# Kernel optimization log

Measured on AMD Instinct MI355X. Metric: run time of the kernel, lower is better.

The kernel has to match this reference:

```python
import jax, jax.numpy as jnp
import numpy as np

B, T, D, H, L, P = 256, 96, 64, 256, 5, 14
H2 = 2 * H   # decoder hidden
O = D        # output_size must equal input_size (decoder feeds its own output back)


def setup_inputs() -> dict:
    key = jax.random.key(0)
    ks = iter(jax.random.split(key, 32))
    s = 0.08  # weight scale to keep gates out of saturation
    rn = lambda shape, sc=s: jax.random.normal(next(ks), shape, jnp.float32) * sc
    return dict(
        x=rn((B, T, D), 1.0),
        # encoder: bidirectional, layer 0 input=D, layers 1..4 input=2H
        enc_Wih0=rn((2, 4 * H, D)), enc_Whh0=rn((2, 4 * H, H)),
        enc_bih0=rn((2, 4 * H)), enc_bhh0=rn((2, 4 * H)),
        enc_Wih=rn((L - 1, 2, 4 * H, 2 * H)), enc_Whh=rn((L - 1, 2, 4 * H, H)),
        enc_bih=rn((L - 1, 2, 4 * H)), enc_bhh=rn((L - 1, 2, 4 * H)),
        # decoder: unidirectional, hidden=2H, layer 0 input=D, layers 1..4 input=2H
        dec_Wih0=rn((4 * H2, D)), dec_Whh0=rn((4 * H2, H2)),
        dec_bih0=rn((4 * H2,)), dec_bhh0=rn((4 * H2,)),
        dec_Wih=rn((L - 1, 4 * H2, H2)), dec_Whh=rn((L - 1, 4 * H2, H2)),
        dec_bih=rn((L - 1, 4 * H2)), dec_bhh=rn((L - 1, 4 * H2)),
        fc_W=rn((O, H2)), fc_b=rn((O,)),
    )


def _lstm_cell(x, h, c, Wih, Whh, bih, bhh):
    # PyTorch gate order: i, f, g, o
    g = x @ Wih.T + h @ Whh.T + (bih + bhh)
    i, f, gg, o = jnp.split(g, 4, axis=-1)
    c = jax.nn.sigmoid(f) * c + jax.nn.sigmoid(i) * jnp.tanh(gg)
    h = jax.nn.sigmoid(o) * jnp.tanh(c)
    return h, c


def _scan_dir(xs, Wih, Whh, bih, bhh, reverse):
    # xs: (T, B, Din); returns per-step hidden (T,B,Hn) + final (h, c)
    Bn, Hn = xs.shape[1], Whh.shape[-1]
    z = jnp.zeros((Bn, Hn), xs.dtype)

    def step(carry, xt):
        h, c = carry
        h, c = _lstm_cell(xt, h, c, Wih, Whh, bih, bhh)
        return (h, c), h

    (hT, cT), hs = jax.lax.scan(step, (z, z), xs, reverse=reverse)
    return hs, hT, cT


def _forward(x, enc_Wih0, enc_Whh0, enc_bih0, enc_bhh0,
             enc_Wih, enc_Whh, enc_bih, enc_bhh,
             dec_Wih0, dec_Whh0, dec_bih0, dec_bhh0,
             dec_Wih, dec_Whh, dec_bih, dec_bhh, fc_W, fc_b):
    xs = jnp.swapaxes(x, 0, 1)  # (T, B, D)
    inp = xs
    h_fin, c_fin = [], []
    for l in range(L):
        if l == 0:
            Wih, Whh, bih, bhh = enc_Wih0, enc_Whh0, enc_bih0, enc_bhh0
        else:
            Wih, Whh, bih, bhh = enc_Wih[l - 1], enc_Whh[l - 1], enc_bih[l - 1], enc_bhh[l - 1]
        hs_f, hTf, cTf = _scan_dir(inp, Wih[0], Whh[0], bih[0], bhh[0], False)
        hs_b, hTb, cTb = _scan_dir(inp, Wih[1], Whh[1], bih[1], bhh[1], True)
        inp = jnp.concatenate([hs_f, hs_b], axis=-1)  # (T, B, 2H)
        # matches h_n.view(L,2,B,H).transpose(1,2).view(L,B,2H): per layer [fwd, bwd]
        h_fin.append(jnp.concatenate([hTf, hTb], axis=-1))
        c_fin.append(jnp.concatenate([cTf, cTb], axis=-1))
    h0 = jnp.stack(h_fin)  # (L, B, 2H)
    c0 = jnp.stack(c_fin)

    dec_params = [(dec_Wih0, dec_Whh0, dec_bih0, dec_bhh0)] + \
                 [(dec_Wih[l], dec_Whh[l], dec_bih[l], dec_bhh[l]) for l in range(L - 1)]

    def dec_step(carry, _):
        h, c, xt = carry
        z = xt
        nh, nc = [], []
        for l, (Wih, Whh, bih, bhh) in enumerate(dec_params):
            hl, cl = _lstm_cell(z, h[l], c[l], Wih, Whh, bih, bhh)
            z = hl
            nh.append(hl); nc.append(cl)
        out = z @ fc_W.T + fc_b  # (B, O); fed back as next decoder input
        return (jnp.stack(nh), jnp.stack(nc), out), out

    _, outs = jax.lax.scan(dec_step, (h0, c0, x[:, -1, :]), None, length=P)
    return jnp.swapaxes(outs, 0, 1)  # (B, P, O)


def reference(x, enc_Wih0, enc_Whh0, enc_bih0, enc_bhh0,
              enc_Wih, enc_Whh, enc_bih, enc_bhh,
              dec_Wih0, dec_Whh0, dec_bih0, dec_bhh0,
              dec_Wih, dec_Whh, dec_bih, dec_bhh, fc_W, fc_b):
    return _forward(x, enc_Wih0, enc_Whh0, enc_bih0, enc_bhh0,
                    enc_Wih, enc_Whh, enc_bih, enc_bhh,
                    dec_Wih0, dec_Whh0, dec_bih0, dec_bhh0,
                    dec_Wih, dec_Whh, dec_bih, dec_bhh, fc_W, fc_b)
```

## Files before the change

kernel.cpp:

```cpp
#include <hip/hip_runtime.h>

typedef _Float16 f16;
using half8 = __attribute__((ext_vector_type(8))) _Float16;
using half4 = __attribute__((ext_vector_type(4))) _Float16;
using f32x4 = __attribute__((ext_vector_type(4))) float;

#define DEV __device__ __forceinline__
#define LD8(p) (*(const half8*)(const void*)(p))

DEV f32x4 mfma16(half8 a, half8 b, f32x4 c) {
  return __builtin_amdgcn_mfma_f32_16x16x32_f16(a, b, c, 0, 0, 0);
}
DEV float sigf(float x) { return 1.f / (1.f + __expf(-x)); }
DEV float tanhf2(float x) { float e = __expf(2.f * x); return 1.f - 2.f / (e + 1.f); }

static const size_t OFF_WIH0   = 0;
static const size_t OFF_WIH14  = 262144;
static const size_t OFF_WHH    = 8650752;
static const size_t OFF_WDEC0  = 13893632;
static const size_t OFF_WDEC14 = 16252928;
static const size_t OFF_WFC    = 33030144;
static const size_t OFF_X16    = 33095680;
static const size_t OFF_SEQA   = 36241408;
static const size_t OFF_SEQB   = 61407232;
static const size_t OFF_XG     = 86573056;
static const size_t OFF_HBUF   = 187236352;
static const size_t OFF_FLAGS  = 187760640;
static const size_t OFF_DHDB   = 188284928;
static const size_t OFF_DCST   = 190906368;
static const size_t OFF_ZFC    = 193527808;

__global__ __launch_bounds__(256) void prep(
    const float* __restrict__ x,
    const float* __restrict__ eWih0, const float* __restrict__ eWhh0,
    const float* __restrict__ eWih,  const float* __restrict__ eWhh,
    const float* __restrict__ dWih0, const float* __restrict__ dWhh0,
    const float* __restrict__ dWih,  const float* __restrict__ dWhh,
    const float* __restrict__ fcW,   char* __restrict__ ws)
{
  f16* wih0   = (f16*)(ws + OFF_WIH0);
  f16* wih14  = (f16*)(ws + OFF_WIH14);
  f16* whhf   = (f16*)(ws + OFF_WHH);
  f16* wdec0  = (f16*)(ws + OFF_WDEC0);
  f16* wdec14 = (f16*)(ws + OFF_WDEC14);
  f16* wfc    = (f16*)(ws + OFF_WFC);
  f16* x16    = (f16*)(ws + OFF_X16);
  f16* zfc    = (f16*)(ws + OFF_ZFC);
  int* flags  = (int*)(ws + OFF_FLAGS);
  const size_t total = 18137344;
  for (size_t i = (size_t)blockIdx.x * blockDim.x + threadIdx.x; i < total;
       i += (size_t)gridDim.x * blockDim.x) {
    size_t j = i;
    if (j < 131072) { wih0[j] = (f16)eWih0[j]; continue; }
    j -= 131072;
    if (j < 4194304) { wih14[j] = (f16)eWih[j]; continue; }
    j -= 4194304;
    if (j < 2621440) {
      size_t l = j >> 19, i2 = j & 524287;
      int d   = (int)(i2 >> 18);
      int uo  = (int)((i2 >> 15) & 7);
      int tile= (int)((i2 >> 14) & 1);
      int g   = (int)((i2 >> 12) & 3);
      int kc  = (int)((i2 >> 9) & 7);
      int lnv = (int)((i2 >> 3) & 63);
      int e   = (int)(i2 & 7);
      int unit = uo * 32 + tile * 16 + (lnv & 15);
      int k = kc * 32 + (lnv >> 4) * 8 + e;
      int row = g * 256 + unit;
      float v = (l == 0) ? eWhh0[((size_t)d * 1024 + row) * 256 + k]
                         : eWhh[((((l - 1) * 2 + (size_t)d) * 1024) + row) * 256 + k];
      whhf[j] = (f16)v;
      continue;
    }
    j -= 2621440;
    if (j < 1179648) {
      size_t r = j / 576, c = j % 576;
      wdec0[j] = (f16)((c < 64) ? dWih0[r * 64 + c] : dWhh0[r * 512 + (c - 64)]);
      continue;
    }
    j -= 1179648;
    if (j < 8388608) {
      size_t l = j >> 21, rem = j & 2097151;
      size_t r = rem >> 10, c = rem & 1023;
      wdec14[j] = (f16)((c < 512) ? dWih[(l * 2048 + r) * 512 + c]
                                  : dWhh[(l * 2048 + r) * 512 + (c - 512)]);
      continue;
    }
    j -= 8388608;
    if (j < 32768) { wfc[j] = (f16)fcW[j]; continue; }
    j -= 32768;
    if (j < 1572864) {
      size_t t = j >> 14, rem = j & 16383;
      size_t b = rem >> 6, d = rem & 63;
      x16[j] = (f16)x[(b * 96 + t) * 64 + d];
      continue;
    }
    j -= 1572864;
    if (j < 16384) {
      size_t b = j >> 6, d = j & 63;
      zfc[b * 512 + d] = (f16)x[(b * 96 + 95) * 64 + d];
      continue;
    }
    j -= 16384;
    flags[j] = 0;
  }
}

__global__ __launch_bounds__(256) void gemm_xg(
    const f16* __restrict__ A, int K, const f16* __restrict__ W,
    const float* __restrict__ bih, const float* __restrict__ bhh,
    f16* __restrict__ xg)
{
  __shared__ __align__(16) f16 As[128 * 32];
  __shared__ __align__(16) f16 Ws[128 * 32];
  const int dir = blockIdx.y >> 3;
  const int cb  = (blockIdx.y & 7) * 128;
  const int rb  = blockIdx.x * 128;
  const int tid = threadIdx.x;
  const int wv = tid >> 6, ln = tid & 63;
  const int wr = wv >> 1, wc = wv & 1;
  const f16* Wd = W + (size_t)dir * 1024 * K;

  f32x4 acc[4][4];
#pragma unroll
  for (int m = 0; m < 4; m++)
#pragma unroll
    for (int n = 0; n < 4; n++) acc[m][n] = (f32x4){0.f, 0.f, 0.f, 0.f};

  const int sr = tid >> 1;
  const int sk = (tid & 1) * 16;
  const int nk = K >> 5;
  for (int kt = 0; kt < nk; ++kt) {
    half8 va0 = LD8(&A[(size_t)(rb + sr) * K + kt * 32 + sk]);
    half8 va1 = LD8(&A[(size_t)(rb + sr) * K + kt * 32 + sk + 8]);
    half8 vw0 = LD8(&Wd[(size_t)(cb + sr) * K + kt * 32 + sk]);
    half8 vw1 = LD8(&Wd[(size_t)(cb + sr) * K + kt * 32 + sk + 8]);
    *(half8*)&As[sr * 32 + sk] = va0;
    *(half8*)&As[sr * 32 + sk + 8] = va1;
    *(half8*)&Ws[sr * 32 + sk] = vw0;
    *(half8*)&Ws[sr * 32 + sk + 8] = vw1;
    __syncthreads();
    half8 af[4], bf[4];
#pragma unroll
    for (int m = 0; m < 4; m++)
      af[m] = LD8(&As[(wr * 64 + m * 16 + (ln & 15)) * 32 + (ln >> 4) * 8]);
#pragma unroll
    for (int n = 0; n < 4; n++)
      bf[n] = LD8(&Ws[(wc * 64 + n * 16 + (ln & 15)) * 32 + (ln >> 4) * 8]);
#pragma unroll
    for (int m = 0; m < 4; m++)
#pragma unroll
      for (int n = 0; n < 4; n++) acc[m][n] = mfma16(af[m], bf[n], acc[m][n]);
    __syncthreads();
  }
#pragma unroll
  for (int n = 0; n < 4; n++) {
    const int col = cb + wc * 64 + n * 16 + (ln & 15);
    const float bsum = bih[dir * 1024 + col] + bhh[dir * 1024 + col];
    const int c16 = (cb + wc * 64 + n * 16) >> 4;
#pragma unroll
    for (int m = 0; m < 4; m++) {
      const int r16 = (rb + wr * 64 + m * 16) >> 4;
      half4 h;
#pragma unroll
      for (int r = 0; r < 4; r++) h[r] = (f16)(acc[m][n][r] + bsum);
      *(half4*)&xg[(((size_t)dir * 1536 + r16) * 64 + c16) * 256 + ln * 4] = h;
    }
  }
}

__global__ __launch_bounds__(128) void enc_layer(
    const f16* __restrict__ xg, const f16* __restrict__ whhf,
    f16* __restrict__ hbuf, int* __restrict__ flags,
    f16* __restrict__ seqo, f16* __restrict__ hfin, float* __restrict__ cfin,
    int layer)
{
  const int bb = blockIdx.x;
  const int d = blockIdx.y >> 3, uo = blockIdx.y & 7;
  const int tid = threadIdx.x;
  const int wv = tid >> 6, ln = tid & 63;
  const int lc = ln & 15, lk = ln >> 4;

  __shared__ __align__(16) f16 wL[32768];
  __shared__ __align__(16) f16 hB[16 * 36];

  const f16* wsrc = whhf + (size_t)(d * 8 + uo) * 32768;
#pragma unroll 4
  for (int i = 0; i < 32; i++)
    *(half8*)&wL[(i * 128 + tid) * 8] = LD8(&wsrc[(size_t)(i * 128 + tid) * 8]);
  __syncthreads();

  int* gflags = &flags[(bb * 2 + d) * 8];
  int* myflag = &gflags[uo];
  const f16* hgrp = hbuf + (size_t)(bb * 2 + d) * 8192;
  f16* hown = hbuf + (size_t)((bb * 2 + d) * 8 + uo) * 1024;
  const int base = layer * 96;
  const int rowbase = bb * 16;
  const int cu = uo * 32 + wv * 16 + lc;
  const int erow = tid >> 3, eu8 = tid & 7;

  f32x4 cst = (f32x4){0.f, 0.f, 0.f, 0.f};

  for (int t = 0; t < 96; ++t) {
    const int tt = d ? 95 - t : t;
    const int par = (t - 1) & 1, par2 = t & 1;
    const int r16 = tt * 16 + bb;
    half4 xv[4];
#pragma unroll
    for (int g = 0; g < 4; g++)
      xv[g] = *(const half4*)&xg[(((size_t)d * 1536 + r16) * 64 +
                                  (g * 16 + uo * 2 + wv)) * 256 + ln * 4];
    unsigned long long q[8][2];
    if (t > 0) {
      if (tid == 0) {
        unsigned spin = 0;
        for (;;) {
          int mn = 0x7fffffff;
#pragma unroll
          for (int p = 0; p < 8; p++) {
            int f = __hip_atomic_load(&gflags[p], __ATOMIC_RELAXED,
                                      __HIP_MEMORY_SCOPE_AGENT);
            mn = (f < mn) ? f : mn;
          }
          if (mn >= base + t || ++spin > 100000u) break;
          __builtin_amdgcn_s_sleep(1);
        }
      }
      __syncthreads();
#pragma unroll
      for (int j = 0; j < 8; j++) {
        const f16* p = hgrp + (size_t)(j * 2 + par) * 512 + lc * 32 + lk * 8;
        q[j][0] = __hip_atomic_load((const unsigned long long*)p,
                                    __ATOMIC_RELAXED, __HIP_MEMORY_SCOPE_AGENT);
        q[j][1] = __hip_atomic_load((const unsigned long long*)(p + 4),
                                    __ATOMIC_RELAXED, __HIP_MEMORY_SCOPE_AGENT);
      }
    }
    f32x4 acc[4];
#pragma unroll
    for (int g = 0; g < 4; g++)
      acc[g] = (f32x4){(float)xv[g][0], (float)xv[g][1],
                       (float)xv[g][2], (float)xv[g][3]};
    if (t > 0) {
#pragma unroll
      for (int j = 0; j < 8; j++) {
        union { unsigned long long uq[2]; half8 h; } u;
        u.uq[0] = q[j][0]; u.uq[1] = q[j][1];
#pragma unroll
        for (int g = 0; g < 4; g++) {
          half8 b = *(const half8*)&wL[(size_t)(((wv * 4 + g) * 8 + j) * 64 + ln) * 8];
          acc[g] = mfma16(u.h, b, acc[g]);
        }
      }
    }
    f16 hv[4];
#pragma unroll
    for (int r = 0; r < 4; r++) {
      float gi = sigf(acc[0][r]);
      float gf = sigf(acc[1][r]);
      float gg = tanhf2(acc[2][r]);
      float go = sigf(acc[3][r]);
      float cn = gf * cst[r] + gi * gg;
      cst[r] = cn;
      hv[r] = (f16)(go * tanhf2(cn));
    }
#pragma unroll
    for (int r = 0; r < 4; r++)
      hB[(lk * 4 + r) * 36 + wv * 16 + lc] = hv[r];
    __syncthreads();
    unsigned long long v = *(const unsigned long long*)&hB[erow * 36 + eu8 * 4];
    __hip_atomic_store((unsigned long long*)&hown[par2 * 512 + erow * 32 + eu8 * 4],
                       v, __ATOMIC_RELAXED, __HIP_MEMORY_SCOPE_AGENT);
    asm volatile("s_waitcnt vmcnt(0)" ::: "memory");
    __syncthreads();
    if (tid == 0)
      __hip_atomic_store(myflag, base + t + 1, __ATOMIC_RELAXED,
                         __HIP_MEMORY_SCOPE_AGENT);
    *(unsigned long long*)&seqo[(size_t)tt * 131072 +
        (size_t)(rowbase + erow) * 512 + d * 256 + uo * 32 + eu8 * 4] = v;
    if (t == 95) {
      *(unsigned long long*)&hfin[(size_t)(rowbase + erow) * 512 +
                                  d * 256 + uo * 32 + eu8 * 4] = v;
#pragma unroll
      for (int r = 0; r < 4; r++)
        cfin[(size_t)(rowbase + lk * 4 + r) * 512 + d * 256 + cu] = cst[r];
    }
  }
}

__global__ __launch_bounds__(128) void dec_step(
    const f16* __restrict__ A0, int K0, const f16* __restrict__ A1,
    const f16* __restrict__ W, int Kt,
    const float* __restrict__ bih, const float* __restrict__ bhh,
    float* __restrict__ cst, f16* __restrict__ h1)
{
  const int u0 = blockIdx.y * 32;
  const int rb = blockIdx.x * 64;
  const int wv = threadIdx.x >> 6, ln = threadIdx.x & 63;
  const int lc = ln & 15, lk = ln >> 4;
  const int cu = u0 + wv * 16 + lc;
  f32x4 acc[4][4];
#pragma unroll
  for (int g = 0; g < 4; g++) {
    float b = bih[g * 512 + cu] + bhh[g * 512 + cu];
#pragma unroll
    for (int rr = 0; rr < 4; rr++) acc[rr][g] = (f32x4){b, b, b, b};
  }
  const int K0c = K0 >> 5, Ktc = Kt >> 5;
  for (int kc = 0; kc < Ktc; kc++) {
    const f16* Ap; int ko;
    if (kc < K0c) { Ap = A0; ko = kc * 32; }
    else          { Ap = A1; ko = (kc - K0c) * 32; }
    half8 b[4];
#pragma unroll
    for (int g = 0; g < 4; g++)
      b[g] = LD8(&W[(size_t)(g * 512 + cu) * Kt + kc * 32 + lk * 8]);
#pragma unroll
    for (int rr = 0; rr < 4; rr++) {
      half8 a = LD8(&Ap[(size_t)(rb + rr * 16 + lc) * 512 + ko + lk * 8]);
#pragma unroll
      for (int g = 0; g < 4; g++) acc[rr][g] = mfma16(a, b[g], acc[rr][g]);
    }
  }
#pragma unroll
  for (int rr = 0; rr < 4; rr++) {
#pragma unroll
    for (int r = 0; r < 4; r++) {
      const int row = rb + rr * 16 + lk * 4 + r;
      float gi = sigf(acc[rr][0][r]);
      float gf = sigf(acc[rr][1][r]);
      float gg = tanhf2(acc[rr][2][r]);
      float go = sigf(acc[rr][3][r]);
      float cp = cst[(size_t)row * 512 + cu];
      float cn = gf * cp + gi * gg;
      cst[(size_t)row * 512 + cu] = cn;
      h1[(size_t)row * 512 + cu] = (f16)(go * tanhf2(cn));
    }
  }
}

__global__ __launch_bounds__(64) void fc_kernel(
    const f16* __restrict__ hin, const f16* __restrict__ Wf,
    const float* __restrict__ bf, float* __restrict__ out,
    f16* __restrict__ zfc, int s)
{
  const int rb = blockIdx.x * 16;
  const int ln = threadIdx.x;
  f32x4 acc[4];
#pragma unroll
  for (int n = 0; n < 4; n++) acc[n] = (f32x4){0.f, 0.f, 0.f, 0.f};
#pragma unroll
  for (int kc = 0; kc < 16; kc++) {
    half8 a = LD8(&hin[(size_t)(rb + (ln & 15)) * 512 + kc * 32 + (ln >> 4) * 8]);
#pragma unroll
    for (int n = 0; n < 4; n++) {
      half8 b = LD8(&Wf[(size_t)(n * 16 + (ln & 15)) * 512 + kc * 32 + (ln >> 4) * 8]);
      acc[n] = mfma16(a, b, acc[n]);
    }
  }
#pragma unroll
  for (int n = 0; n < 4; n++) {
    const int col = n * 16 + (ln & 15);
    const float bb = bf[col];
#pragma unroll
    for (int r = 0; r < 4; r++) {
      const int row = rb + (ln >> 4) * 4 + r;
      float v = acc[n][r] + bb;
      out[(size_t)row * 896 + s * 64 + col] = v;
      zfc[(size_t)row * 512 + col] = (f16)v;
    }
  }
}

extern "C" void kernel_launch(void* const* d_in, const int* in_sizes, int n_in,
                              void* d_out, int out_size, void* d_ws, size_t ws_size,
                              hipStream_t stream) {
  char* ws = (char*)d_ws;
  const float* x     = (const float*)d_in[0];
  const float* eWih0 = (const float*)d_in[1];
  const float* eWhh0 = (const float*)d_in[2];
  const float* ebih0 = (const float*)d_in[3];
  const float* ebhh0 = (const float*)d_in[4];
  const float* eWih  = (const float*)d_in[5];
  const float* eWhh  = (const float*)d_in[6];
  const float* ebih  = (const float*)d_in[7];
  const float* ebhh  = (const float*)d_in[8];
  const float* dWih0 = (const float*)d_in[9];
  const float* dWhh0 = (const float*)d_in[10];
  const float* dbih0 = (const float*)d_in[11];
  const float* dbhh0 = (const float*)d_in[12];
  const float* dWih  = (const float*)d_in[13];
  const float* dWhh  = (const float*)d_in[14];
  const float* dbih  = (const float*)d_in[15];
  const float* dbhh  = (const float*)d_in[16];
  const float* fcW   = (const float*)d_in[17];
  const float* fcb   = (const float*)d_in[18];

  f16* xg    = (f16*)(ws + OFF_XG);
  f16* hbuf  = (f16*)(ws + OFF_HBUF);
  int* flags = (int*)(ws + OFF_FLAGS);
  f16* dhdb  = (f16*)(ws + OFF_DHDB);
  float* dcst = (float*)(ws + OFF_DCST);
  f16* zfc   = (f16*)(ws + OFF_ZFC);
  f16* seqA  = (f16*)(ws + OFF_SEQA);
  f16* seqB  = (f16*)(ws + OFF_SEQB);

  prep<<<dim3(2048), dim3(256), 0, stream>>>(x, eWih0, eWhh0, eWih, eWhh,
                                             dWih0, dWhh0, dWih, dWhh, fcW, ws);

  for (int l = 0; l < 5; ++l) {
    const f16* Ain = (l == 0) ? (f16*)(ws + OFF_X16) : ((l & 1) ? seqA : seqB);
    const int K = (l == 0) ? 64 : 512;
    const f16* Wih = (l == 0) ? (f16*)(ws + OFF_WIH0)
                              : (f16*)(ws + OFF_WIH14) + (size_t)(l - 1) * 2 * 1024 * 512;
    const float* bi = (l == 0) ? ebih0 : ebih + (size_t)(l - 1) * 2048;
    const float* bh = (l == 0) ? ebhh0 : ebhh + (size_t)(l - 1) * 2048;
    gemm_xg<<<dim3(192, 16), dim3(256), 0, stream>>>(Ain, K, Wih, bi, bh, xg);

    const f16* whhf_l = (f16*)(ws + OFF_WHH) + (size_t)l * 524288;
    f16* so = (l & 1) ? seqB : seqA;
    enc_layer<<<dim3(16, 16), dim3(128), 0, stream>>>(
        xg, whhf_l, hbuf, flags, so,
        dhdb + (size_t)l * 131072, dcst + (size_t)l * 131072, l);
  }

  for (int s = 0; s < 14; ++s) {
    const int p = s & 1;
    for (int l = 0; l < 5; ++l) {
      dec_step<<<dim3(4, 16), dim3(128), 0, stream>>>(
          (l == 0) ? zfc : dhdb + (size_t)(p ^ 1) * 655360 + (size_t)(l - 1) * 131072,
          (l == 0) ? 64 : 512,
          dhdb + (size_t)p * 655360 + (size_t)l * 131072,
          (l == 0) ? (f16*)(ws + OFF_WDEC0)
                   : (f16*)(ws + OFF_WDEC14) + (size_t)(l - 1) * 2048 * 1024,
          (l == 0) ? 576 : 1024,
          (l == 0) ? dbih0 : dbih + (size_t)(l - 1) * 2048,
          (l == 0) ? dbhh0 : dbhh + (size_t)(l - 1) * 2048,
          dcst + (size_t)l * 131072,
          dhdb + (size_t)(p ^ 1) * 655360 + (size_t)l * 131072);
    }
    fc_kernel<<<dim3(16), dim3(64), 0, stream>>>(
        dhdb + (size_t)(p ^ 1) * 655360 + 4 * 131072, (f16*)(ws + OFF_WFC), fcb,
        (float*)d_out, zfc, s);
  }
}
```

Measured before the change: 3.863 ms.

## Replace flag-based step barrier with tagged hidden-state words in encoder

The encoder recurrent kernel stops publishing a per-block flag after each timestep and spinning on peer flags. Instead, every f16 hidden value is stored in a 32-bit word whose high half carries the timestep tag, and consumers spin directly on the data until all tags match. This removes the waitcnt, the extra barrier and the flag round trip on the critical path of each step. In exchange it doubles the hidden-state exchange traffic, makes every lane poll 32 words, and drops the flag initialisation. Stale words from earlier layers or runs cannot match because the tag encodes layer times 96 plus t.

```diff
diff --git a/kernel.cpp b/kernel.cpp
--- a/kernel.cpp
+++ b/kernel.cpp
@@ -25,7 +25,6 @@
 static const size_t OFF_SEQB   = 61407232;
 static const size_t OFF_XG     = 86573056;
 static const size_t OFF_HBUF   = 187236352;
-static const size_t OFF_FLAGS  = 187760640;
 static const size_t OFF_DHDB   = 188284928;
 static const size_t OFF_DCST   = 190906368;
 static const size_t OFF_ZFC    = 193527808;
@@ -46,8 +45,7 @@
   f16* wfc    = (f16*)(ws + OFF_WFC);
   f16* x16    = (f16*)(ws + OFF_X16);
   f16* zfc    = (f16*)(ws + OFF_ZFC);
-  int* flags  = (int*)(ws + OFF_FLAGS);
-  const size_t total = 18137344;
+  const size_t total = 18137088;
   for (size_t i = (size_t)blockIdx.x * blockDim.x + threadIdx.x; i < total;
        i += (size_t)gridDim.x * blockDim.x) {
     size_t j = i;
@@ -96,13 +94,10 @@
       continue;
     }
     j -= 1572864;
-    if (j < 16384) {
+    {
       size_t b = j >> 6, d = j & 63;
       zfc[b * 512 + d] = (f16)x[(b * 96 + 95) * 64 + d];
-      continue;
-    }
-    j -= 16384;
-    flags[j] = 0;
+    }
   }
 }
 
@@ -171,7 +166,7 @@
 
 __global__ __launch_bounds__(128) void enc_layer(
     const f16* __restrict__ xg, const f16* __restrict__ whhf,
-    f16* __restrict__ hbuf, int* __restrict__ flags,
+    unsigned* __restrict__ hbuf,
     f16* __restrict__ seqo, f16* __restrict__ hfin, float* __restrict__ cfin,
     int layer)
 {
@@ -190,14 +185,11 @@
     *(half8*)&wL[(i * 128 + tid) * 8] = LD8(&wsrc[(size_t)(i * 128 + tid) * 8]);
   __syncthreads();
 
-  int* gflags = &flags[(bb * 2 + d) * 8];
-  int* myflag = &gflags[uo];
-  const f16* hgrp = hbuf + (size_t)(bb * 2 + d) * 8192;
-  f16* hown = hbuf + (size_t)((bb * 2 + d) * 8 + uo) * 1024;
+  unsigned* hbase = hbuf + (size_t)(bb * 2 + d) * 8192;
   const int base = layer * 96;
   const int rowbase = bb * 16;
   const int cu = uo * 32 + wv * 16 + lc;
-  const int erow = tid >> 3, eu8 = tid & 7;
+  const int erow = tid >> 3, e4 = (tid & 7) * 4;
 
   f32x4 cst = (f32x4){0.f, 0.f, 0.f, 0.f};
 
@@ -210,42 +202,41 @@
     for (int g = 0; g < 4; g++)
       xv[g] = *(const half4*)&xg[(((size_t)d * 1536 + r16) * 64 +
                                   (g * 16 + uo * 2 + wv)) * 256 + ln * 4];
-    unsigned long long q[8][2];
-    if (t > 0) {
-      if (tid == 0) {
-        unsigned spin = 0;
-        for (;;) {
-          int mn = 0x7fffffff;
-#pragma unroll
-          for (int p = 0; p < 8; p++) {
-            int f = __hip_atomic_load(&gflags[p], __ATOMIC_RELAXED,
-                                      __HIP_MEMORY_SCOPE_AGENT);
-            mn = (f < mn) ? f : mn;
-          }
-          if (mn >= base + t || ++spin > 100000u) break;
-          __builtin_amdgcn_s_sleep(1);
-        }
-      }
-      __syncthreads();
-#pragma unroll
-      for (int j = 0; j < 8; j++) {
-        const f16* p = hgrp + (size_t)(j * 2 + par) * 512 + lc * 32 + lk * 8;
-        q[j][0] = __hip_atomic_load((const unsigned long long*)p,
-                                    __ATOMIC_RELAXED, __HIP_MEMORY_SCOPE_AGENT);
-        q[j][1] = __hip_atomic_load((const unsigned long long*)(p + 4),
-                                    __ATOMIC_RELAXED, __HIP_MEMORY_SCOPE_AGENT);
-      }
-    }
     f32x4 acc[4];
 #pragma unroll
     for (int g = 0; g < 4; g++)
       acc[g] = (f32x4){(float)xv[g][0], (float)xv[g][1],
                        (float)xv[g][2], (float)xv[g][3]};
+
     if (t > 0) {
+      const unsigned tagexp = (unsigned)(base + t - 1);
+      const unsigned long long* hrow = (const unsigned long long*)
+          (hbase + ((size_t)par * 16 + lc) * 256);
+      unsigned long long q[32];
+      unsigned spin = 0;
+      bool ok;
+      do {
+        ok = true;
+#pragma unroll
+        for (int j = 0; j < 8; j++) {
+          const unsigned long long* p = hrow + (j * 32 + lk * 8) / 2;
+#pragma unroll
+          for (int m = 0; m < 4; m++) {
+            q[j * 4 + m] = __hip_atomic_load(p + m, __ATOMIC_RELAXED,
+                                             __HIP_MEMORY_SCOPE_AGENT);
+            ok = ok && ((((unsigned)q[j * 4 + m]) >> 16) == tagexp);
+          }
+        }
+      } while (!ok && ++spin < 50000u);
 #pragma unroll
       for (int j = 0; j < 8; j++) {
-        union { unsigned long long uq[2]; half8 h; } u;
-        u.uq[0] = q[j][0]; u.uq[1] = q[j][1];
+        union { unsigned w[4]; half8 h; } u;
+#pragma unroll
+        for (int m = 0; m < 4; m++) {
+          unsigned long long qq = q[j * 4 + m];
+          u.w[m] = ((unsigned)qq & 0xFFFFu) |
+                   ((((unsigned)(qq >> 32)) & 0xFFFFu) << 16);
+        }
 #pragma unroll
         for (int g = 0; g < 4; g++) {
           half8 b = *(const half8*)&wL[(size_t)(((wv * 4 + g) * 8 + j) * 64 + ln) * 8];
@@ -268,23 +259,30 @@
     for (int r = 0; r < 4; r++)
       hB[(lk * 4 + r) * 36 + wv * 16 + lc] = hv[r];
     __syncthreads();
-    unsigned long long v = *(const unsigned long long*)&hB[erow * 36 + eu8 * 4];
-    __hip_atomic_store((unsigned long long*)&hown[par2 * 512 + erow * 32 + eu8 * 4],
-                       v, __ATOMIC_RELAXED, __HIP_MEMORY_SCOPE_AGENT);
-    asm volatile("s_waitcnt vmcnt(0)" ::: "memory");
+    {
+      const unsigned tagv = (unsigned)(base + t) << 16;
+      unsigned long long v = *(const unsigned long long*)&hB[erow * 36 + e4];
+      unsigned lo = (unsigned)v, hi = (unsigned)(v >> 32);
+      unsigned long long t0 = (unsigned long long)((lo & 0xFFFFu) | tagv) |
+                              ((unsigned long long)((lo >> 16) | tagv) << 32);
+      unsigned long long t1 = (unsigned long long)((hi & 0xFFFFu) | tagv) |
+                              ((unsigned long long)((hi >> 16) | tagv) << 32);
+      unsigned* hdst = hbase + ((size_t)par2 * 16 + erow) * 256 + uo * 32 + e4;
+      __hip_atomic_store((unsigned long long*)hdst, t0,
+                         __ATOMIC_RELAXED, __HIP_MEMORY_SCOPE_AGENT);
+      __hip_atomic_store((unsigned long long*)(hdst + 2), t1,
+                         __ATOMIC_RELAXED, __HIP_MEMORY_SCOPE_AGENT);
+      *(unsigned long long*)&seqo[(size_t)tt * 131072 +
+          (size_t)(rowbase + erow) * 512 + d * 256 + uo * 32 + e4] = v;
+      if (t == 95) {
+        *(unsigned long long*)&hfin[(size_t)(rowbase + erow) * 512 +
+                                    d * 256 + uo * 32 + e4] = v;
+#pragma unroll
+        for (int r = 0; r < 4; r++)
+          cfin[(size_t)(rowbase + lk * 4 + r) * 512 + d * 256 + cu] = cst[r];
+      }
+    }
     __syncthreads();
-    if (tid == 0)
-      __hip_atomic_store(myflag, base + t + 1, __ATOMIC_RELAXED,
-                         __HIP_MEMORY_SCOPE_AGENT);
-    *(unsigned long long*)&seqo[(size_t)tt * 131072 +
-        (size_t)(rowbase + erow) * 512 + d * 256 + uo * 32 + eu8 * 4] = v;
-    if (t == 95) {
-      *(unsigned long long*)&hfin[(size_t)(rowbase + erow) * 512 +
-                                  d * 256 + uo * 32 + eu8 * 4] = v;
-#pragma unroll
-      for (int r = 0; r < 4; r++)
-        cfin[(size_t)(rowbase + lk * 4 + r) * 512 + d * 256 + cu] = cst[r];
-    }
   }
 }
 
@@ -397,8 +395,7 @@
   const float* fcb   = (const float*)d_in[18];
 
   f16* xg    = (f16*)(ws + OFF_XG);
-  f16* hbuf  = (f16*)(ws + OFF_HBUF);
-  int* flags = (int*)(ws + OFF_FLAGS);
+  unsigned* hbuf = (unsigned*)(ws + OFF_HBUF);
   f16* dhdb  = (f16*)(ws + OFF_DHDB);
   float* dcst = (float*)(ws + OFF_DCST);
   f16* zfc   = (f16*)(ws + OFF_ZFC);
@@ -420,7 +417,7 @@
     const f16* whhf_l = (f16*)(ws + OFF_WHH) + (size_t)l * 524288;
     f16* so = (l & 1) ? seqB : seqA;
     enc_layer<<<dim3(16, 16), dim3(128), 0, stream>>>(
-        xg, whhf_l, hbuf, flags, so,
+        xg, whhf_l, hbuf, so,
         dhdb + (size_t)l * 131072, dcst + (size_t)l * 131072, l);
   }
 
```

After: 4.047 ms. 1.05x slower.
